# Kernel optimization log

Hardware: AMD Instinct MI355X
Metric: run time of the kernel (lower is better)

## Reference

```python
import jax, jax.numpy as jnp
import numpy as np

EPS = 1e-5
TEMP = 0.07
LARGE_NEG = -1e9


def mi_net(x, W1, g1, b1, W2, b2, Ws, lng, lnb):
    # x: (B, C, T). 1x1 convs == per-position channel projections.
    y = jnp.einsum('bct,oc->bot', x, W1)                      # conv1 (no bias)
    mu = y.mean(axis=(0, 2), keepdims=True)                   # BatchNorm2d, training-mode batch stats
    var = y.var(axis=(0, 2), keepdims=True)
    y = (y - mu) * jax.lax.rsqrt(var + EPS) * g1[None, :, None] + b1[None, :, None]
    y = jax.nn.relu(y)
    y = jnp.einsum('bot,po->bpt', y, W2) + b2[None, :, None]  # conv2 (bias)
    h = y + jnp.einsum('bct,oc->bot', x, Ws)                  # linear shortcut
    mu2 = h.mean(axis=1, keepdims=True)                       # LayerNorm over channel dim
    v2 = h.var(axis=1, keepdims=True)
    return (h - mu2) * jax.lax.rsqrt(v2 + EPS) * lng[None, :, None] + lnb[None, :, None]


def infonce(L, G):
    # L: (N, D, T) locals, G: (N, D) single global per sample (n_multis = 1)
    N, D, T = L.shape
    l_p = jnp.swapaxes(L, 1, 2)                               # (N, T, D)
    l_p = l_p / jnp.linalg.norm(l_p, axis=2, keepdims=True)
    g = G / jnp.linalg.norm(G, axis=1, keepdims=True)         # (N, D)
    u_p = (jnp.einsum('ntd,nd->nt', l_p, g) / TEMP)[:, :, None]   # (N, T, 1), positives scaled by temp
    # negatives: <global_i, local_{j,t}>; NOT divided by temperature (faithful to torch source)
    u_n = jnp.einsum('nd,mtd->nmt', g, l_p)                   # (N, N, T)
    eye = jnp.eye(N, dtype=bool)[:, :, None]
    u_n = jnp.where(eye, LARGE_NEG, u_n).reshape(N, N * T)    # mask self pairs
    logits = jnp.concatenate(
        [u_p, jnp.broadcast_to(u_n[:, None, :], (N, T, N * T))], axis=2)  # (N, T, 1+N*T)
    logp = jax.nn.log_softmax(logits, axis=2)
    return -logp[:, :, 0].mean()


def setup_inputs() -> dict:
    key = jax.random.key(0)
    ks = jax.random.split(key, 10)
    B, CL, CG, T, MI = 32, 1536, 192, 256, 512
    d = {
        'local_feat': jax.random.normal(ks[0], (B, CL, T), jnp.float32),
        'global_feat': jax.random.normal(ks[1], (B, CG), jnp.float32),
        # local_net params
        'lW1': jax.random.normal(ks[2], (MI, CL), jnp.float32) * 0.02,
        'lg1': jnp.ones((MI,), jnp.float32),
        'lb1': jnp.zeros((MI,), jnp.float32),
        'lW2': jax.random.normal(ks[3], (MI, MI), jnp.float32) * 0.02,
        'lb2': jnp.zeros((MI,), jnp.float32),
        'lWs': jax.random.normal(ks[4], (MI, CL), jnp.float32) * 0.02,
        'llng': jnp.ones((MI,), jnp.float32),
        'llnb': jnp.zeros((MI,), jnp.float32),
        # global_net params (global_channels != mi_units -> net exists)
        'gW1': jax.random.normal(ks[5], (MI, CG), jnp.float32) * 0.02,
        'gg1': jnp.ones((MI,), jnp.float32),
        'gb1': jnp.zeros((MI,), jnp.float32),
        'gW2': jax.random.normal(ks[6], (MI, MI), jnp.float32) * 0.02,
        'gb2': jnp.zeros((MI,), jnp.float32),
    }
    # shortcut with near-identity init (n_units >= n_input for global net)
    gWs = jax.random.uniform(ks[7], (MI, CG), jnp.float32, -0.01, 0.01)
    gWs = gWs.at[jnp.arange(CG), jnp.arange(CG)].set(1.0)
    d['gWs'] = gWs
    d['glng'] = jnp.ones((MI,), jnp.float32)
    d['glnb'] = jnp.zeros((MI,), jnp.float32)
    return d


def reference(local_feat, global_feat,
              lW1, lg1, lb1, lW2, lb2, lWs, llng, llnb,
              gW1, gg1, gb1, gW2, gb2, gWs, glng, glnb):
    L = mi_net(local_feat, lW1, lg1, lb1, lW2, lb2, lWs, llng, llnb)      # (B, MI, T)
    G = mi_net(global_feat[:, :, None], gW1, gg1, gb1, gW2, gb2, gWs, glng, glnb)[:, :, 0]  # (B, MI)
    return infonce(L, G)
```

## Files before the change

kernel.cpp:

```cpp
#include <hip/hip_runtime.h>

#define B 32
#define CL 1536
#define CG 192
#define T 256
#define MI 512
#define NPOS 8192
#define EPS 1e-5f
#define TEMP 0.07f

typedef __attribute__((ext_vector_type(8))) __bf16 bf16x8;
typedef __attribute__((ext_vector_type(4))) float f32x4;

__device__ __forceinline__ unsigned short f2bf(float f) {
  union { float f; unsigned u; } v; v.f = f;
  unsigned r = v.u + 0x7FFFu + ((v.u >> 16) & 1u);
  return (unsigned short)(r >> 16);
}
__device__ __forceinline__ float bf2f(unsigned short h) {
  union { unsigned u; float f; } v; v.u = ((unsigned)h) << 16;
  return v.f;
}

__device__ __forceinline__ float wave_sum(float v) {
#pragma unroll
  for (int off = 32; off > 0; off >>= 1) v += __shfl_xor(v, off, 64);
  return v;
}
__device__ __forceinline__ float block_sum(float v, float* rb) {
  v = wave_sum(v);
  __syncthreads();
  if ((threadIdx.x & 63) == 0) rb[threadIdx.x >> 6] = v;
  __syncthreads();
  return rb[0] + rb[1] + rb[2] + rb[3];
}
__device__ __forceinline__ float bs128(float v, float* rb) {
  v = wave_sum(v);
  __syncthreads();
  if ((threadIdx.x & 63) == 0) rb[threadIdx.x >> 6] = v;
  __syncthreads();
  return rb[0] + rb[1];
}

__global__ __launch_bounds__(256) void k_prep(
    const float* __restrict__ x, const float* __restrict__ lW1,
    const float* __restrict__ lWs, const float* __restrict__ lW2,
    const float* __restrict__ gx, const float* __restrict__ gW1,
    unsigned short* __restrict__ xT, unsigned short* __restrict__ Wc,
    unsigned short* __restrict__ W2b, float* __restrict__ y1g,
    float* __restrict__ bsum) {
  __shared__ float xs[64][65];
  const int bi = blockIdx.x, tid = threadIdx.x;
  if (bi < 1792) {
    int idx = (bi * 256 + tid) * 4;
    const float* src; unsigned short* dst;
    if (idx < 786432) { src = lW1 + idx; dst = Wc + idx; }
    else if (idx < 1572864) { src = lWs + (idx - 786432); dst = Wc + idx; }
    else { src = lW2 + (idx - 1572864); dst = W2b + (idx - 1572864); }
    float4 v = *(const float4*)src;
    ushort4 o = {f2bf(v.x), f2bf(v.y), f2bf(v.z), f2bf(v.w)};
    *(ushort4*)dst = o;
  } else if (bi < 4864) {
    int bi2 = bi - 1792;
    int b = bi2 / 96, rem = bi2 - b * 96;
    int c0 = (rem >> 2) * 64, t0 = (rem & 3) * 64;
    const float* xb = x + ((size_t)b * CL + c0) * T + t0;
#pragma unroll
    for (int i = 0; i < 16; i++) {
      int idx = tid + i * 256, c = idx >> 6, t = idx & 63;
      xs[c][t] = xb[(size_t)c * T + t];
    }
    __syncthreads();
    unsigned short* ob = xT + ((size_t)b * T + t0) * CL + c0;
#pragma unroll
    for (int half = 0; half < 2; half++) {
      int s = tid + half * 256;
      int t = s >> 3, kg = s & 7;
      unsigned short v[8];
#pragma unroll
      for (int j = 0; j < 8; j++) v[j] = f2bf(xs[kg * 8 + j][t]);
      uint4 o = {(unsigned)v[0] | ((unsigned)v[1] << 16),
                 (unsigned)v[2] | ((unsigned)v[3] << 16),
                 (unsigned)v[4] | ((unsigned)v[5] << 16),
                 (unsigned)v[6] | ((unsigned)v[7] << 16)};
      *(uint4*)&ob[(size_t)t * CL + kg * 8] = o;
    }
  } else if (bi < 4928) {
    int idx = (bi - 4864) * 256 + tid;
    int b = idx & 31, o = idx >> 5;
    float s = 0.f;
    for (int c = 0; c < CG; c++) s = fmaf(gx[b * CG + c], gW1[o * CG + c], s);
    y1g[o * 32 + b] = s;
  } else {
    float4 z = {0.f, 0.f, 0.f, 0.f};
    ((float4*)bsum)[tid] = z;
  }
}

__global__ __launch_bounds__(128, 2) void k_gemm1(
    const unsigned short* __restrict__ xT, const unsigned short* __restrict__ Wc,
    unsigned short* __restrict__ y1u, unsigned short* __restrict__ ysb,
    float* __restrict__ bsum, float* __restrict__ bsq,
    const float* __restrict__ y1g, const float* __restrict__ gg1,
    const float* __restrict__ gb1, const float* __restrict__ gW2,
    const float* __restrict__ gb2, const float* __restrict__ gx,
    const float* __restrict__ gWsc, float* __restrict__ hg) {
  const int tid = threadIdx.x, bi = blockIdx.x;
  if (bi >= 1024) {
    __shared__ float gsc[512], gsh[512];
#pragma unroll
    for (int jj = 0; jj < 4; jj++) {
      int o = tid + jj * 128;
      float s = 0.f, s2 = 0.f;
      for (int b = 0; b < 32; b++) {
        float v = y1g[o * 32 + b];
        s += v; s2 = fmaf(v, v, s2);
      }
      float mu = s * (1.f / 32.f);
      float var = s2 * (1.f / 32.f) - mu * mu;
      float sc = gg1[o] * rsqrtf(var + EPS);
      gsc[o] = sc;
      gsh[o] = gb1[o] - mu * sc;
    }
    __syncthreads();
    int base = (bi - 1024) * 256;
#pragma unroll
    for (int jj = 0; jj < 2; jj++) {
      int idx = base + jj * 128 + tid;
      int b = idx & 31, p = idx >> 5;
      float s = gb2[p];
      for (int o = 0; o < MI; o++) {
        float v = fmaxf(fmaf(y1g[o * 32 + b], gsc[o], gsh[o]), 0.f);
        s = fmaf(v, gW2[(size_t)p * MI + o], s);
      }
      for (int c = 0; c < CG; c++) s = fmaf(gx[b * CG + c], gWsc[p * CG + c], s);
      hg[p * 32 + b] = s;
    }
    return;
  }
  __shared__ __align__(16) unsigned short As[64 * 64];
  __shared__ __align__(16) unsigned short Bs[128 * 64];
  __shared__ float ps[128], pq[128];
  const int w = tid >> 6, lane = tid & 63;
  const int m0 = (bi & 127) * 64, o0 = (bi >> 7) * 128;
  const int r8 = lane >> 3;
  const int csw = ((lane & 7) ^ r8) * 8;
  const int lm = lane & 15, q = lane >> 4;
  const int sw0 = lm & 7;
  f32x4 acc[4][4];
#pragma unroll
  for (int i = 0; i < 4; i++)
#pragma unroll
    for (int j = 0; j < 4; j++) acc[i][j] = f32x4{0.f, 0.f, 0.f, 0.f};

  const unsigned short* pa = xT + (size_t)(m0 + w * 32 + r8) * CL + csw;
  const unsigned short* pb = Wc + (size_t)(o0 + w * 64 + r8) * CL + csw;
  for (int k0 = 0; k0 < CL; k0 += 64) {
#pragma unroll
    for (int i = 0; i < 4; i++)
      __builtin_amdgcn_global_load_lds(
          (const __attribute__((address_space(1))) void*)(pa + (size_t)i * 8 * CL + k0),
          (__attribute__((address_space(3))) void*)&As[(w * 32 + i * 8) * 64], 16, 0, 0);
#pragma unroll
    for (int i = 0; i < 8; i++)
      __builtin_amdgcn_global_load_lds(
          (const __attribute__((address_space(1))) void*)(pb + (size_t)i * 8 * CL + k0),
          (__attribute__((address_space(3))) void*)&Bs[(w * 64 + i * 8) * 64], 16, 0, 0);
    __syncthreads();
#pragma unroll
    for (int kc = 0; kc < 2; kc++) {
      const int ch = ((kc * 4 + q) ^ sw0) * 8;
      bf16x8 af[4], bfr[4];
#pragma unroll
      for (int mi = 0; mi < 4; mi++)
        af[mi] = *(const bf16x8*)&As[(mi * 16 + lm) * 64 + ch];
#pragma unroll
      for (int ni = 0; ni < 4; ni++)
        bfr[ni] = *(const bf16x8*)&Bs[(w * 64 + ni * 16 + lm) * 64 + ch];
#pragma unroll
      for (int mi = 0; mi < 4; mi++)
#pragma unroll
        for (int ni = 0; ni < 4; ni++)
          acc[mi][ni] = __builtin_amdgcn_mfma_f32_16x16x32_bf16(
              af[mi], bfr[ni], acc[mi][ni], 0, 0, 0);
    }
    __syncthreads();
  }
  const int row0 = m0 + q * 4;
  const bool isY1 = (o0 < 512);
  unsigned short* dst = isY1 ? y1u : ysb;
  const int ob = isY1 ? o0 : o0 - 512;
#pragma unroll
  for (int mi = 0; mi < 4; mi++)
#pragma unroll
    for (int ni = 0; ni < 4; ni++) {
      int oc = ob + w * 64 + ni * 16 + lm;
#pragma unroll
      for (int r = 0; r < 4; r++)
        dst[(size_t)(row0 + mi * 16 + r) * 512 + oc] = f2bf(acc[mi][ni][r]);
    }
  if (isY1) {
#pragma unroll
    for (int ni = 0; ni < 4; ni++) {
      float s = 0.f, s2 = 0.f;
#pragma unroll
      for (int mi = 0; mi < 4; mi++)
#pragma unroll
        for (int r = 0; r < 4; r++) {
          float v = acc[mi][ni][r];
          s += v; s2 = fmaf(v, v, s2);
        }
      s += __shfl_xor(s, 16, 64);  s2 += __shfl_xor(s2, 16, 64);
      s += __shfl_xor(s, 32, 64);  s2 += __shfl_xor(s2, 32, 64);
      if (q == 0) {
        int c = w * 64 + ni * 16 + lm;
        ps[c] = s; pq[c] = s2;
      }
    }
    __syncthreads();
    atomicAdd(&bsum[o0 + tid], ps[tid]);
    atomicAdd(&bsq[o0 + tid], pq[tid]);
  }
}

__global__ __launch_bounds__(128, 2) void k_gemm2(
    const unsigned short* __restrict__ y1u, const unsigned short* __restrict__ W2b,
    const float* __restrict__ bsum, const float* __restrict__ bsq,
    const float* __restrict__ lg1, const float* __restrict__ lb1,
    const float* __restrict__ b2, unsigned short* __restrict__ hb16,
    const float* __restrict__ hg, const float* __restrict__ glng,
    const float* __restrict__ glnb, unsigned short* __restrict__ gnormb) {
  __shared__ __align__(16) unsigned short As[64 * 64];
  __shared__ __align__(16) unsigned short Bs[128 * 64];
  __shared__ float scl[512], shf[512];
  __shared__ float rb[2];
  const int tid = threadIdx.x, bi = blockIdx.x;
  if (bi >= 512) {
    int b = bi - 512;
    float v[4], Lv[4];
    float s = 0.f, s2 = 0.f;
#pragma unroll
    for (int j = 0; j < 4; j++) {
      v[j] = hg[(tid + j * 128) * 32 + b];
      s += v[j]; s2 = fmaf(v[j], v[j], s2);
    }
    s = bs128(s, rb);
    s2 = bs128(s2, rb);
    float mu = s * (1.f / MI);
    float var = s2 * (1.f / MI) - mu * mu;
    float rstd = rsqrtf(var + EPS);
    float n2 = 0.f;
#pragma unroll
    for (int j = 0; j < 4; j++) {
      int p = tid + j * 128;
      Lv[j] = fmaf((v[j] - mu) * rstd, glng[p], glnb[p]);
      n2 = fmaf(Lv[j], Lv[j], n2);
    }
    n2 = bs128(n2, rb);
    float inv = rsqrtf(n2);
#pragma unroll
    for (int j = 0; j < 4; j++)
      gnormb[b * MI + tid + j * 128] = f2bf(Lv[j] * inv);
    return;
  }
  const int w = tid >> 6, lane = tid & 63;
  const int m0 = (bi & 127) * 64, p0 = (bi >> 7) * 128;
  const int r8 = lane >> 3;
  const int csw = ((lane & 7) ^ r8) * 8;
  const int lm = lane & 15, q = lane >> 4;
  const int sw0 = lm & 7;
#pragma unroll
  for (int jj = 0; jj < 4; jj++) {
    int ch = tid + jj * 128;
    float mu = bsum[ch] * (1.f / NPOS);
    float var = bsq[ch] * (1.f / NPOS) - mu * mu;
    float sc = lg1[ch] * rsqrtf(var + EPS);
    scl[ch] = sc;
    shf[ch] = lb1[ch] - mu * sc;
  }
  __syncthreads();
  f32x4 acc[4][4];
#pragma unroll
  for (int i = 0; i < 4; i++)
#pragma unroll
    for (int j = 0; j < 4; j++) acc[i][j] = f32x4{0.f, 0.f, 0.f, 0.f};

  const int cg = tid & 7, rbase = tid >> 3;
  const unsigned short* pb = W2b + (size_t)(p0 + w * 64 + r8) * 512 + csw;
  for (int k0 = 0; k0 < 512; k0 += 64) {
#pragma unroll
    for (int i = 0; i < 8; i++)
      __builtin_amdgcn_global_load_lds(
          (const __attribute__((address_space(1))) void*)(pb + (size_t)i * 8 * 512 + k0),
          (__attribute__((address_space(3))) void*)&Bs[(w * 64 + i * 8) * 64], 16, 0, 0);
    float sreg[8], hreg[8];
#pragma unroll
    for (int j = 0; j < 8; j++) {
      sreg[j] = scl[k0 + cg * 8 + j];
      hreg[j] = shf[k0 + cg * 8 + j];
    }
#pragma unroll
    for (int pass = 0; pass < 4; pass++) {
      int row = rbase + pass * 16;
      uint4 u = *(const uint4*)&y1u[(size_t)(m0 + row) * 512 + k0 + cg * 8];
      unsigned short iv[8] = {
          (unsigned short)(u.x & 0xffff), (unsigned short)(u.x >> 16),
          (unsigned short)(u.y & 0xffff), (unsigned short)(u.y >> 16),
          (unsigned short)(u.z & 0xffff), (unsigned short)(u.z >> 16),
          (unsigned short)(u.w & 0xffff), (unsigned short)(u.w >> 16)};
      unsigned short ov[8];
#pragma unroll
      for (int j = 0; j < 8; j++)
        ov[j] = f2bf(fmaxf(fmaf(bf2f(iv[j]), sreg[j], hreg[j]), 0.f));
      uint4 o = {(unsigned)ov[0] | ((unsigned)ov[1] << 16),
                 (unsigned)ov[2] | ((unsigned)ov[3] << 16),
                 (unsigned)ov[4] | ((unsigned)ov[5] << 16),
                 (unsigned)ov[6] | ((unsigned)ov[7] << 16)};
      *(uint4*)&As[row * 64 + ((cg ^ (row & 7)) * 8)] = o;
    }
    __syncthreads();
#pragma unroll
    for (int kc = 0; kc < 2; kc++) {
      const int ch = ((kc * 4 + q) ^ sw0) * 8;
      bf16x8 af[4], bfr[4];
#pragma unroll
      for (int mi = 0; mi < 4; mi++)
        af[mi] = *(const bf16x8*)&As[(mi * 16 + lm) * 64 + ch];
#pragma unroll
      for (int ni = 0; ni < 4; ni++)
        bfr[ni] = *(const bf16x8*)&Bs[(w * 64 + ni * 16 + lm) * 64 + ch];
#pragma unroll
      for (int mi = 0; mi < 4; mi++)
#pragma unroll
        for (int ni = 0; ni < 4; ni++)
          acc[mi][ni] = __builtin_amdgcn_mfma_f32_16x16x32_bf16(
              af[mi], bfr[ni], acc[mi][ni], 0, 0, 0);
    }
    __syncthreads();
  }
  const int row0 = m0 + q * 4;
#pragma unroll
  for (int ni = 0; ni < 4; ni++) {
    int p = p0 + w * 64 + ni * 16 + lm;
    float bias = b2[p];
#pragma unroll
    for (int mi = 0; mi < 4; mi++)
#pragma unroll
      for (int r = 0; r < 4; r++) {
        size_t off = (size_t)(row0 + mi * 16 + r) * 512 + p;
        hb16[off] = f2bf(acc[mi][ni][r] + bias);
      }
  }
}

__global__ __launch_bounds__(256) void k_tail(
    const unsigned short* __restrict__ hb16, const unsigned short* __restrict__ ysb,
    const float* __restrict__ lng, const float* __restrict__ lnb,
    const unsigned short* __restrict__ gnormb,
    float* __restrict__ up, float* __restrict__ pmax, float* __restrict__ psum) {
  __shared__ __align__(16) unsigned short gs[32 * 512];
  __shared__ __align__(16) unsigned short Ls[32 * 512];
  __shared__ float Ured[4 * 1024];
  const int tid = threadIdx.x;
  const int w = tid >> 6, lane = tid & 63;
  const int r0 = blockIdx.x * 32;
  const int smp = r0 >> 8;
#pragma unroll
  for (int i = 0; i < 8; i++) {
    int e = (tid + i * 256) * 8;
    *(uint4*)&gs[e] = *(const uint4*)&gnormb[e];
  }
  float4 g0 = *(const float4*)&lng[lane * 8];
  float4 g1 = *(const float4*)&lng[lane * 8 + 4];
  float4 bb0 = *(const float4*)&lnb[lane * 8];
  float4 bb1 = *(const float4*)&lnb[lane * 8 + 4];
  float gg[8] = {g0.x, g0.y, g0.z, g0.w, g1.x, g1.y, g1.z, g1.w};
  float bz[8] = {bb0.x, bb0.y, bb0.z, bb0.w, bb1.x, bb1.y, bb1.z, bb1.w};
#pragma unroll
  for (int j = 0; j < 8; j++) {
    int rr = w * 8 + j;
    size_t off = (size_t)(r0 + rr) * 512 + lane * 8;
    uint4 hu = *(const uint4*)&hb16[off];
    uint4 yu = *(const uint4*)&ysb[off];
    unsigned short hv[8] = {
        (unsigned short)(hu.x & 0xffff), (unsigned short)(hu.x >> 16),
        (unsigned short)(hu.y & 0xffff), (unsigned short)(hu.y >> 16),
        (unsigned short)(hu.z & 0xffff), (unsigned short)(hu.z >> 16),
        (unsigned short)(hu.w & 0xffff), (unsigned short)(hu.w >> 16)};
    unsigned short yv[8] = {
        (unsigned short)(yu.x & 0xffff), (unsigned short)(yu.x >> 16),
        (unsigned short)(yu.y & 0xffff), (unsigned short)(yu.y >> 16),
        (unsigned short)(yu.z & 0xffff), (unsigned short)(yu.z >> 16),
        (unsigned short)(yu.w & 0xffff), (unsigned short)(yu.w >> 16)};
    float v[8];
    float s = 0.f, s2 = 0.f;
#pragma unroll
    for (int k = 0; k < 8; k++) {
      v[k] = bf2f(hv[k]) + bf2f(yv[k]);
      s += v[k]; s2 = fmaf(v[k], v[k], s2);
    }
    s = wave_sum(s);
    s2 = wave_sum(s2);
    float mu = s * (1.f / MI);
    float var = s2 * (1.f / MI) - mu * mu;
    float rstd = rsqrtf(var + EPS);
    float L[8], n2 = 0.f;
#pragma unroll
    for (int k = 0; k < 8; k++) {
      L[k] = fmaf((v[k] - mu) * rstd, gg[k], bz[k]);
      n2 = fmaf(L[k], L[k], n2);
    }
    n2 = wave_sum(n2);
    float inv = rsqrtf(n2);
    unsigned short* orow = &Ls[rr * 512 + lane * 8];
    ushort4 o0 = {f2bf(L[0] * inv), f2bf(L[1] * inv), f2bf(L[2] * inv), f2bf(L[3] * inv)};
    ushort4 o1 = {f2bf(L[4] * inv), f2bf(L[5] * inv), f2bf(L[6] * inv), f2bf(L[7] * inv)};
    *(ushort4*)orow = o0;
    *(ushort4*)(orow + 4) = o1;
  }
  __syncthreads();
  const int lm = lane & 15, q = lane >> 4;
  f32x4 acc[2][2];
#pragma unroll
  for (int i = 0; i < 2; i++)
#pragma unroll
    for (int j = 0; j < 2; j++) acc[i][j] = f32x4{0.f, 0.f, 0.f, 0.f};
#pragma unroll
  for (int kk = 0; kk < 4; kk++) {
    int k0 = w * 128 + kk * 32 + q * 8;
    bf16x8 af[2], bfr[2];
#pragma unroll
    for (int mi = 0; mi < 2; mi++)
      af[mi] = *(const bf16x8*)&gs[(mi * 16 + lm) * 512 + k0];
#pragma unroll
    for (int ni = 0; ni < 2; ni++)
      bfr[ni] = *(const bf16x8*)&Ls[(ni * 16 + lm) * 512 + k0];
#pragma unroll
    for (int mi = 0; mi < 2; mi++)
#pragma unroll
      for (int ni = 0; ni < 2; ni++)
        acc[mi][ni] = __builtin_amdgcn_mfma_f32_16x16x32_bf16(
            af[mi], bfr[ni], acc[mi][ni], 0, 0, 0);
  }
#pragma unroll
  for (int mi = 0; mi < 2; mi++)
#pragma unroll
    for (int ni = 0; ni < 2; ni++)
#pragma unroll
      for (int r = 0; r < 4; r++) {
        int m = mi * 16 + q * 4 + r, n = ni * 16 + lm;
        Ured[w * 1024 + m * 32 + n] = acc[mi][ni][r];
      }
  __syncthreads();
  float u[4];
#pragma unroll
  for (int j = 0; j < 4; j++) {
    int idx = tid * 4 + j;
    u[j] = Ured[idx] + Ured[1024 + idx] + Ured[2048 + idx] + Ured[3072 + idx];
  }
  __syncthreads();
#pragma unroll
  for (int j = 0; j < 4; j++) Ured[tid * 4 + j] = u[j];
  int m = (tid * 4) >> 5;
  if (m == smp) {
#pragma unroll
    for (int j = 0; j < 4; j++)
      up[r0 + ((tid * 4 + j) & 31)] = u[j] * (1.f / TEMP);
  }
  __syncthreads();
  if (tid < 32) {
    float mx = -1e30f, s = 0.f;
    if (tid != smp) {
      for (int n = 0; n < 32; n++) mx = fmaxf(mx, Ured[tid * 32 + n]);
      for (int n = 0; n < 32; n++) s += expf(Ured[tid * 32 + n] - mx);
    }
    pmax[tid * 256 + blockIdx.x] = mx;
    psum[tid * 256 + blockIdx.x] = s;
  }
}

__global__ __launch_bounds__(256) void k_loss(
    const float* __restrict__ up, const float* __restrict__ pmax,
    const float* __restrict__ psum, float* __restrict__ out) {
  __shared__ float rb[4];
  __shared__ float red[32][8];
  __shared__ float Ms[32], Ss[32];
  const int tid = threadIdx.x;
  const int n = tid >> 3, j = tid & 7;
  float mx = -1e30f;
  for (int c = j * 32; c < j * 32 + 32; c++) mx = fmaxf(mx, pmax[n * 256 + c]);
  red[n][j] = mx;
  __syncthreads();
  if (j == 0) {
    float M = -1e30f;
#pragma unroll
    for (int k = 0; k < 8; k++) M = fmaxf(M, red[n][k]);
    Ms[n] = M;
  }
  __syncthreads();
  float M = Ms[n];
  float s = 0.f;
  for (int c = j * 32; c < j * 32 + 32; c++)
    s += psum[n * 256 + c] * expf(pmax[n * 256 + c] - M);
  __syncthreads();
  red[n][j] = s;
  __syncthreads();
  if (j == 0) {
    float S = 0.f;
#pragma unroll
    for (int k = 0; k < 8; k++) S += red[n][k];
    Ss[n] = S;
  }
  __syncthreads();
  float acc = 0.f;
  for (int i = tid; i < NPOS; i += 256) {
    int nn = i >> 8;
    float upv = up[i];
    float Mn = Ms[nn], Sn = Ss[nn];
    float mx2 = fmaxf(upv, Mn);
    float lse = mx2 + logf(expf(upv - mx2) + Sn * expf(Mn - mx2));
    acc += lse - upv;
  }
  acc = block_sum(acc, rb);
  if (tid == 0) out[0] = acc * (1.f / NPOS);
}

extern "C" void kernel_launch(void* const* d_in, const int* in_sizes, int n_in,
                              void* d_out, int out_size, void* d_ws, size_t ws_size,
                              hipStream_t stream) {
  (void)in_sizes; (void)n_in; (void)out_size; (void)ws_size;
  const float* x    = (const float*)d_in[0];
  const float* gx   = (const float*)d_in[1];
  const float* lW1  = (const float*)d_in[2];
  const float* lg1  = (const float*)d_in[3];
  const float* lb1  = (const float*)d_in[4];
  const float* lW2  = (const float*)d_in[5];
  const float* lb2  = (const float*)d_in[6];
  const float* lWs  = (const float*)d_in[7];
  const float* llng = (const float*)d_in[8];
  const float* llnb = (const float*)d_in[9];
  const float* gW1  = (const float*)d_in[10];
  const float* gg1  = (const float*)d_in[11];
  const float* gb1  = (const float*)d_in[12];
  const float* gW2  = (const float*)d_in[13];
  const float* gb2  = (const float*)d_in[14];
  const float* gWs  = (const float*)d_in[15];
  const float* glng = (const float*)d_in[16];
  const float* glnb = (const float*)d_in[17];

  char* wsb = (char*)d_ws;
  unsigned short* xT     = (unsigned short*)(wsb);
  unsigned short* Wc     = (unsigned short*)(wsb + 25165824);
  unsigned short* W2b    = (unsigned short*)(wsb + 28311552);
  unsigned short* y1u    = (unsigned short*)(wsb + 28835840);
  unsigned short* ysb    = (unsigned short*)(wsb + 37224448);
  unsigned short* hb16   = (unsigned short*)(wsb + 54001664);
  float* bsum            = (float*)(wsb + 71827456);
  float* bsq             = (float*)(wsb + 71829504);
  float* y1g             = (float*)(wsb + 71831552);
  float* hg              = (float*)(wsb + 71901184);
  unsigned short* gnormb = (unsigned short*)(wsb + 71966720);
  float* up              = (float*)(wsb + 71999488);
  float* pmax            = (float*)(wsb + 72032256);
  float* psum            = (float*)(wsb + 72065024);

  k_prep<<<dim3(4929), 256, 0, stream>>>(x, lW1, lWs, lW2, gx, gW1, xT, Wc, W2b,
                                         y1g, bsum);
  k_gemm1<<<dim3(1088), 128, 0, stream>>>(xT, Wc, y1u, ysb, bsum, bsq,
                                          y1g, gg1, gb1, gW2, gb2, gx, gWs, hg);
  k_gemm2<<<dim3(544), 128, 0, stream>>>(y1u, W2b, bsum, bsq, lg1, lb1, lb2,
                                         hb16, hg, glng, glnb, gnormb);
  k_tail<<<dim3(256), 256, 0, stream>>>(hb16, ysb, llng, llnb, gnormb,
                                        up, pmax, psum);
  k_loss<<<dim3(1), 256, 0, stream>>>(up, pmax, psum, (float*)d_out);
}
```

Before: 233.7 us.

## Load GEMM operands directly from global into registers, dropping LDS staging

Both MFMA GEMM kernels stop staging tiles through LDS with barriers. Each wave now loads its A/B fragments straight from global memory into registers and double-buffers them across even and odd k-halves. gemm1 moves to 256-thread blocks covering a 128x128 tile and issues per-lane atomics for the batch-norm statistics. gemm2 applies the BN scale/shift and ReLU in registers on the loaded fragments. This removes LDS traffic and syncs, but operands are no longer shared between waves, so global/L2 traffic rises and the per-lane fragment loads are strided across rows.

Result: slower. 288.9 us (+23.6%).

```diff
diff --git a/kernel.cpp b/kernel.cpp
--- a/kernel.cpp
+++ b/kernel.cpp
@@ -97,7 +97,7 @@
   }
 }
 
-__global__ __launch_bounds__(128, 2) void k_gemm1(
+__global__ __launch_bounds__(256, 2) void k_gemm1(
     const unsigned short* __restrict__ xT, const unsigned short* __restrict__ Wc,
     unsigned short* __restrict__ y1u, unsigned short* __restrict__ ysb,
     float* __restrict__ bsum, float* __restrict__ bsq,
@@ -106,11 +106,11 @@
     const float* __restrict__ gb2, const float* __restrict__ gx,
     const float* __restrict__ gWsc, float* __restrict__ hg) {
   const int tid = threadIdx.x, bi = blockIdx.x;
-  if (bi >= 1024) {
+  if (bi >= 512) {
     __shared__ float gsc[512], gsh[512];
 #pragma unroll
-    for (int jj = 0; jj < 4; jj++) {
-      int o = tid + jj * 128;
+    for (int jj = 0; jj < 2; jj++) {
+      int o = tid + jj * 256;
       float s = 0.f, s2 = 0.f;
       for (int b = 0; b < 32; b++) {
         float v = y1g[o * 32 + b];
@@ -123,78 +123,68 @@
       gsh[o] = gb1[o] - mu * sc;
     }
     __syncthreads();
-    int base = (bi - 1024) * 256;
-#pragma unroll
-    for (int jj = 0; jj < 2; jj++) {
-      int idx = base + jj * 128 + tid;
-      int b = idx & 31, p = idx >> 5;
-      float s = gb2[p];
-      for (int o = 0; o < MI; o++) {
-        float v = fmaxf(fmaf(y1g[o * 32 + b], gsc[o], gsh[o]), 0.f);
-        s = fmaf(v, gW2[(size_t)p * MI + o], s);
-      }
-      for (int c = 0; c < CG; c++) s = fmaf(gx[b * CG + c], gWsc[p * CG + c], s);
-      hg[p * 32 + b] = s;
-    }
+    int idx = (bi - 512) * 256 + tid;
+    int b = idx & 31, p = idx >> 5;
+    float s = gb2[p];
+    for (int o = 0; o < MI; o++) {
+      float v = fmaxf(fmaf(y1g[o * 32 + b], gsc[o], gsh[o]), 0.f);
+      s = fmaf(v, gW2[(size_t)p * MI + o], s);
+    }
+    for (int c = 0; c < CG; c++) s = fmaf(gx[b * CG + c], gWsc[p * CG + c], s);
+    hg[p * 32 + b] = s;
     return;
   }
-  __shared__ __align__(16) unsigned short As[64 * 64];
-  __shared__ __align__(16) unsigned short Bs[128 * 64];
-  __shared__ float ps[128], pq[128];
   const int w = tid >> 6, lane = tid & 63;
-  const int m0 = (bi & 127) * 64, o0 = (bi >> 7) * 128;
-  const int r8 = lane >> 3;
-  const int csw = ((lane & 7) ^ r8) * 8;
   const int lm = lane & 15, q = lane >> 4;
-  const int sw0 = lm & 7;
+  const int m0 = (bi >> 3) * 128 + (w & 1) * 64;
+  const int n0 = (bi & 7) * 128 + (w >> 1) * 64;
+  const unsigned short* pA = xT + (size_t)(m0 + lm) * CL + q * 8;
+  const unsigned short* pB = Wc + (size_t)(n0 + lm) * CL + q * 8;
   f32x4 acc[4][4];
 #pragma unroll
   for (int i = 0; i < 4; i++)
 #pragma unroll
     for (int j = 0; j < 4; j++) acc[i][j] = f32x4{0.f, 0.f, 0.f, 0.f};
 
-  const unsigned short* pa = xT + (size_t)(m0 + w * 32 + r8) * CL + csw;
-  const unsigned short* pb = Wc + (size_t)(o0 + w * 64 + r8) * CL + csw;
+  bf16x8 Ae[4], Be[4], Ao[4], Bo[4];
+#pragma unroll
+  for (int i = 0; i < 4; i++) {
+    Ae[i] = *(const bf16x8*)(pA + (size_t)i * 16 * CL);
+    Be[i] = *(const bf16x8*)(pB + (size_t)i * 16 * CL);
+  }
   for (int k0 = 0; k0 < CL; k0 += 64) {
 #pragma unroll
-    for (int i = 0; i < 4; i++)
-      __builtin_amdgcn_global_load_lds(
-          (const __attribute__((address_space(1))) void*)(pa + (size_t)i * 8 * CL + k0),
-          (__attribute__((address_space(3))) void*)&As[(w * 32 + i * 8) * 64], 16, 0, 0);
-#pragma unroll
-    for (int i = 0; i < 8; i++)
-      __builtin_amdgcn_global_load_lds(
-          (const __attribute__((address_space(1))) void*)(pb + (size_t)i * 8 * CL + k0),
-          (__attribute__((address_space(3))) void*)&Bs[(w * 64 + i * 8) * 64], 16, 0, 0);
-    __syncthreads();
-#pragma unroll
-    for (int kc = 0; kc < 2; kc++) {
-      const int ch = ((kc * 4 + q) ^ sw0) * 8;
-      bf16x8 af[4], bfr[4];
-#pragma unroll
-      for (int mi = 0; mi < 4; mi++)
-        af[mi] = *(const bf16x8*)&As[(mi * 16 + lm) * 64 + ch];
+    for (int i = 0; i < 4; i++) {
+      Ao[i] = *(const bf16x8*)(pA + (size_t)i * 16 * CL + k0 + 32);
+      Bo[i] = *(const bf16x8*)(pB + (size_t)i * 16 * CL + k0 + 32);
+    }
+#pragma unroll
+    for (int mi = 0; mi < 4; mi++)
 #pragma unroll
       for (int ni = 0; ni < 4; ni++)
-        bfr[ni] = *(const bf16x8*)&Bs[(w * 64 + ni * 16 + lm) * 64 + ch];
-#pragma unroll
-      for (int mi = 0; mi < 4; mi++)
-#pragma unroll
-        for (int ni = 0; ni < 4; ni++)
-          acc[mi][ni] = __builtin_amdgcn_mfma_f32_16x16x32_bf16(
-              af[mi], bfr[ni], acc[mi][ni], 0, 0, 0);
-    }
-    __syncthreads();
+        acc[mi][ni] = __builtin_amdgcn_mfma_f32_16x16x32_bf16(
+            Ae[mi], Be[ni], acc[mi][ni], 0, 0, 0);
+#pragma unroll
+    for (int i = 0; i < 4; i++) {
+      Ae[i] = *(const bf16x8*)(pA + (size_t)i * 16 * CL + k0 + 64);
+      Be[i] = *(const bf16x8*)(pB + (size_t)i * 16 * CL + k0 + 64);
+    }
+#pragma unroll
+    for (int mi = 0; mi < 4; mi++)
+#pragma unroll
+      for (int ni = 0; ni < 4; ni++)
+        acc[mi][ni] = __builtin_amdgcn_mfma_f32_16x16x32_bf16(
+            Ao[mi], Bo[ni], acc[mi][ni], 0, 0, 0);
   }
   const int row0 = m0 + q * 4;
-  const bool isY1 = (o0 < 512);
+  const bool isY1 = (n0 < 512);
   unsigned short* dst = isY1 ? y1u : ysb;
-  const int ob = isY1 ? o0 : o0 - 512;
+  const int ob = isY1 ? n0 : n0 - 512;
 #pragma unroll
   for (int mi = 0; mi < 4; mi++)
 #pragma unroll
     for (int ni = 0; ni < 4; ni++) {
-      int oc = ob + w * 64 + ni * 16 + lm;
+      int oc = ob + ni * 16 + lm;
 #pragma unroll
       for (int r = 0; r < 4; r++)
         dst[(size_t)(row0 + mi * 16 + r) * 512 + oc] = f2bf(acc[mi][ni][r]);
@@ -213,13 +203,10 @@
       s += __shfl_xor(s, 16, 64);  s2 += __shfl_xor(s2, 16, 64);
       s += __shfl_xor(s, 32, 64);  s2 += __shfl_xor(s2, 32, 64);
       if (q == 0) {
-        int c = w * 64 + ni * 16 + lm;
-        ps[c] = s; pq[c] = s2;
+        atomicAdd(&bsum[n0 + ni * 16 + lm], s);
+        atomicAdd(&bsq[n0 + ni * 16 + lm], s2);
       }
     }
-    __syncthreads();
-    atomicAdd(&bsum[o0 + tid], ps[tid]);
-    atomicAdd(&bsq[o0 + tid], pq[tid]);
   }
 }
 
@@ -230,8 +217,6 @@
     const float* __restrict__ b2, unsigned short* __restrict__ hb16,
     const float* __restrict__ hg, const float* __restrict__ glng,
     const float* __restrict__ glnb, unsigned short* __restrict__ gnormb) {
-  __shared__ __align__(16) unsigned short As[64 * 64];
-  __shared__ __align__(16) unsigned short Bs[128 * 64];
   __shared__ float scl[512], shf[512];
   __shared__ float rb[2];
   const int tid = threadIdx.x, bi = blockIdx.x;
@@ -263,12 +248,6 @@
       gnormb[b * MI + tid + j * 128] = f2bf(Lv[j] * inv);
     return;
   }
-  const int w = tid >> 6, lane = tid & 63;
-  const int m0 = (bi & 127) * 64, p0 = (bi >> 7) * 128;
-  const int r8 = lane >> 3;
-  const int csw = ((lane & 7) ^ r8) * 8;
-  const int lm = lane & 15, q = lane >> 4;
-  const int sw0 = lm & 7;
 #pragma unroll
   for (int jj = 0; jj < 4; jj++) {
     int ch = tid + jj * 128;
@@ -279,69 +258,86 @@
     shf[ch] = lb1[ch] - mu * sc;
   }
   __syncthreads();
+  const int w = tid >> 6, lane = tid & 63;
+  const int lm = lane & 15, q = lane >> 4;
+  const int m0 = (bi >> 2) * 64;
+  const int p0 = (bi & 3) * 128 + w * 64;
+  const unsigned short* pA = y1u + (size_t)(m0 + lm) * 512 + q * 8;
+  const unsigned short* pB = W2b + (size_t)(p0 + lm) * 512 + q * 8;
   f32x4 acc[4][4];
 #pragma unroll
   for (int i = 0; i < 4; i++)
 #pragma unroll
     for (int j = 0; j < 4; j++) acc[i][j] = f32x4{0.f, 0.f, 0.f, 0.f};
 
-  const int cg = tid & 7, rbase = tid >> 3;
-  const unsigned short* pb = W2b + (size_t)(p0 + w * 64 + r8) * 512 + csw;
+  bf16x8 Ae[4], Be[4], Ao[4], Bo[4];
+#pragma unroll
+  for (int i = 0; i < 4; i++) {
+    Ae[i] = *(const bf16x8*)(pA + (size_t)i * 16 * 512);
+    Be[i] = *(const bf16x8*)(pB + (size_t)i * 16 * 512);
+  }
   for (int k0 = 0; k0 < 512; k0 += 64) {
 #pragma unroll
-    for (int i = 0; i < 8; i++)
-      __builtin_amdgcn_global_load_lds(
-          (const __attribute__((address_space(1))) void*)(pb + (size_t)i * 8 * 512 + k0),
-          (__attribute__((address_space(3))) void*)&Bs[(w * 64 + i * 8) * 64], 16, 0, 0);
-    float sreg[8], hreg[8];
-#pragma unroll
-    for (int j = 0; j < 8; j++) {
-      sreg[j] = scl[k0 + cg * 8 + j];
-      hreg[j] = shf[k0 + cg * 8 + j];
-    }
-#pragma unroll
-    for (int pass = 0; pass < 4; pass++) {
-      int row = rbase + pass * 16;
-      uint4 u = *(const uint4*)&y1u[(size_t)(m0 + row) * 512 + k0 + cg * 8];
-      unsigned short iv[8] = {
-          (unsigned short)(u.x & 0xffff), (unsigned short)(u.x >> 16),
-          (unsigned short)(u.y & 0xffff), (unsigned short)(u.y >> 16),
-          (unsigned short)(u.z & 0xffff), (unsigned short)(u.z >> 16),
-          (unsigned short)(u.w & 0xffff), (unsigned short)(u.w >> 16)};
-      unsigned short ov[8];
-#pragma unroll
-      for (int j = 0; j < 8; j++)
-        ov[j] = f2bf(fmaxf(fmaf(bf2f(iv[j]), sreg[j], hreg[j]), 0.f));
-      uint4 o = {(unsigned)ov[0] | ((unsigned)ov[1] << 16),
-                 (unsigned)ov[2] | ((unsigned)ov[3] << 16),
-                 (unsigned)ov[4] | ((unsigned)ov[5] << 16),
-                 (unsigned)ov[6] | ((unsigned)ov[7] << 16)};
-      *(uint4*)&As[row * 64 + ((cg ^ (row & 7)) * 8)] = o;
-    }
-    __syncthreads();
-#pragma unroll
-    for (int kc = 0; kc < 2; kc++) {
-      const int ch = ((kc * 4 + q) ^ sw0) * 8;
-      bf16x8 af[4], bfr[4];
-#pragma unroll
-      for (int mi = 0; mi < 4; mi++)
-        af[mi] = *(const bf16x8*)&As[(mi * 16 + lm) * 64 + ch];
-#pragma unroll
-      for (int ni = 0; ni < 4; ni++)
-        bfr[ni] = *(const bf16x8*)&Bs[(w * 64 + ni * 16 + lm) * 64 + ch];
+    for (int i = 0; i < 4; i++) {
+      Ao[i] = *(const bf16x8*)(pA + (size_t)i * 16 * 512 + k0 + 32);
+      Bo[i] = *(const bf16x8*)(pB + (size_t)i * 16 * 512 + k0 + 32);
+    }
+    {
+      float sv[8], hv[8];
+      *(float4*)&sv[0] = *(const float4*)&scl[k0 + q * 8];
+      *(float4*)&sv[4] = *(const float4*)&scl[k0 + q * 8 + 4];
+      *(float4*)&hv[0] = *(const float4*)&shf[k0 + q * 8];
+      *(float4*)&hv[4] = *(const float4*)&shf[k0 + q * 8 + 4];
+      bf16x8 af[4];
+#pragma unroll
+      for (int mi = 0; mi < 4; mi++) {
+        union { bf16x8 v; unsigned short u[8]; } in, out;
+        in.v = Ae[mi];
+#pragma unroll
+        for (int j = 0; j < 8; j++)
+          out.u[j] = f2bf(fmaxf(fmaf(bf2f(in.u[j]), sv[j], hv[j]), 0.f));
+        af[mi] = out.v;
+      }
 #pragma unroll
       for (int mi = 0; mi < 4; mi++)
 #pragma unroll
         for (int ni = 0; ni < 4; ni++)
           acc[mi][ni] = __builtin_amdgcn_mfma_f32_16x16x32_bf16(
-              af[mi], bfr[ni], acc[mi][ni], 0, 0, 0);
-    }
-    __syncthreads();
+              af[mi], Be[ni], acc[mi][ni], 0, 0, 0);
+    }
+#pragma unroll
+    for (int i = 0; i < 4; i++) {
+      Ae[i] = *(const bf16x8*)(pA + (size_t)i * 16 * 512 + k0 + 64);
+      Be[i] = *(const bf16x8*)(pB + (size_t)i * 16 * 512 + k0 + 64);
+    }
+    {
+      float sv[8], hv[8];
+      *(float4*)&sv[0] = *(const float4*)&scl[k0 + 32 + q * 8];
+      *(float4*)&sv[4] = *(const float4*)&scl[k0 + 32 + q * 8 + 4];
+      *(float4*)&hv[0] = *(const float4*)&shf[k0 + 32 + q * 8];
+      *(float4*)&hv[4] = *(const float4*)&shf[k0 + 32 + q * 8 + 4];
+      bf16x8 af[4];
+#pragma unroll
+      for (int mi = 0; mi < 4; mi++) {
+        union { bf16x8 v; unsigned short u[8]; } in, out;
+        in.v = Ao[mi];
+#pragma unroll
+        for (int j = 0; j < 8; j++)
+          out.u[j] = f2bf(fmaxf(fmaf(bf2f(in.u[j]), sv[j], hv[j]), 0.f));
+        af[mi] = out.v;
+      }
+#pragma unroll
+      for (int mi = 0; mi < 4; mi++)
+#pragma unroll
+        for (int ni = 0; ni < 4; ni++)
+          acc[mi][ni] = __builtin_amdgcn_mfma_f32_16x16x32_bf16(
+              af[mi], Bo[ni], acc[mi][ni], 0, 0, 0);
+    }
   }
   const int row0 = m0 + q * 4;
 #pragma unroll
   for (int ni = 0; ni < 4; ni++) {
-    int p = p0 + w * 64 + ni * 16 + lm;
+    int p = p0 + ni * 16 + lm;
     float bias = b2[p];
 #pragma unroll
     for (int mi = 0; mi < 4; mi++)
@@ -566,8 +562,8 @@
 
   k_prep<<<dim3(4929), 256, 0, stream>>>(x, lW1, lWs, lW2, gx, gW1, xT, Wc, W2b,
                                          y1g, bsum);
-  k_gemm1<<<dim3(1088), 128, 0, stream>>>(xT, Wc, y1u, ysb, bsum, bsq,
-                                          y1g, gg1, gb1, gW2, gb2, gx, gWs, hg);
+  k_gemm1<<<dim3(576), 256, 0, stream>>>(xT, Wc, y1u, ysb, bsum, bsq,
+                                         y1g, gg1, gb1, gW2, gb2, gx, gWs, hg);
   k_gemm2<<<dim3(544), 128, 0, stream>>>(y1u, W2b, bsum, bsq, lg1, lb1, lb2,
                                          hb16, hg, glng, glnb, gnormb);
   k_tail<<<dim3(256), 256, 0, stream>>>(hb16, ysb, llng, llnb, gnormb,
```
